# Performance work log

Measured on AMD Instinct MI355X. Metric: run time of the kernel, lower is better.

Reference implementation:

```python
import jax, jax.numpy as jnp
import numpy as np


def setup_inputs() -> dict:
    key = jax.random.key(0)
    k1, k2 = jax.random.split(key)
    B, N, M, K = 8, 4096, 4096, 64
    input1 = jax.random.normal(k1, (B, N, K), dtype=jnp.float32)
    input2 = jax.random.normal(k2, (B, M, K), dtype=jnp.float32)
    return {"input1": input1, "input2": input2}


def reference(input1, input2):
    # Pairwise L2 distances via the ||x||^2 + ||y||^2 - 2<x,y> identity,
    # avoiding the O(B*N*M*K) broadcast-subtraction intermediate.
    x2 = jnp.sum(input1 * input1, axis=-1)                 # [B, N]
    y2 = jnp.sum(input2 * input2, axis=-1)                 # [B, M]
    xy = jnp.einsum('bnk,bmk->bnm', input1, input2)        # [B, N, M]
    sq = x2[:, :, None] + y2[:, None, :] - 2.0 * xy
    D = jnp.sqrt(jnp.maximum(sq, 0.0))                     # [B, N, M]
    dist0 = jnp.mean(jnp.min(D, axis=1), axis=1)           # min over N, mean over M
    dist1 = jnp.mean(jnp.min(D, axis=2), axis=1)           # min over M, mean over N
    loss = jnp.mean(dist0 + dist1)
    return loss
```

## Files before the change

### kernel.cpp

```cpp
#include <hip/hip_runtime.h>

#define BATCH 8
#define NPTS  4096
#define KD    64
#define MQ    4
#define WALK  8
#define FINF  3.0e38f

typedef float f32x4 __attribute__((ext_vector_type(4)));
typedef float f32x2 __attribute__((ext_vector_type(2)));
typedef short s16x8 __attribute__((ext_vector_type(8)));

__device__ __forceinline__ unsigned int f2bf(float f) {
  unsigned int u = __float_as_uint(f);
  u += 0x7FFFu + ((u >> 16) & 1u);
  return u >> 16;
}

__device__ __forceinline__ void stage16(const void* g, void* l) {
  __builtin_amdgcn_global_load_lds((const __attribute__((address_space(1))) void*)g,
                                   (__attribute__((address_space(3))) void*)l, 16, 0, 0);
}

__global__ __launch_bounds__(256)
void prep_kernel(const float* __restrict__ X, const float* __restrict__ Y,
                 unsigned int* __restrict__ Xbf, unsigned int* __restrict__ Ybf,
                 float* __restrict__ x2, float* __restrict__ y2,
                 unsigned int* __restrict__ counter) {
  int gid = blockIdx.x * 256 + threadIdx.x;
  if (gid == 0) *counter = 0;
  int row = gid >> 5;
  int ki  = gid & 31;
  bool isX = row < BATCH * NPTS;
  int r2 = row & (BATCH * NPTS - 1);
  const float* src = isX ? X : Y;
  f32x2 v = *(const f32x2*)(src + (size_t)r2 * KD + ki * 2);
  float s = v[0] * v[0] + v[1] * v[1];
  #pragma unroll
  for (int m = 16; m >= 1; m >>= 1) s += __shfl_xor(s, m, 64);
  unsigned int packed = (f2bf(v[1]) << 16) | f2bf(v[0]);
  (isX ? Xbf : Ybf)[r2 * 32 + ki] = packed;
  if (ki == 0) (isX ? x2 : y2)[r2] = s;
}

__global__ __launch_bounds__(256, 2)
void chamfer_main(const unsigned short* __restrict__ Xbf,
                  const unsigned short* __restrict__ Ybf,
                  const float* __restrict__ x2g, const float* __restrict__ y2g,
                  float* __restrict__ rowpart,
                  float* __restrict__ colpart) {
  __shared__ __align__(16) unsigned short Ys[2][128 * 64];
  __shared__ float l_credq[2 * 4 * 132];
  __shared__ float l_redf[256];

  const int mq = blockIdx.x, ntile = blockIdx.y, b = blockIdx.z;
  const int n0 = ntile * 128;
  const int mbase = mq * (WALK * 128);
  const int t = threadIdx.x, w = t >> 6, lane = t & 63, c = lane & 15, q = lane >> 4;
  const int wr = (w >> 1) * 64, wc = (w & 1) * 64, rg = w >> 1;

  const int l8 = lane >> 3;
  const int lane_off = l8 * 128 + (((lane & 7) ^ l8) << 4);

  const unsigned short* Xrow = Xbf + (size_t)(b * NPTS + n0) * KD;
  const char* Yg0 = (const char*)(Ybf + (size_t)(b * NPTS + mbase) * KD);

  #pragma unroll
  for (int k = 0; k < 4; ++k)
    stage16(Yg0 + (k * 32 + w * 8) * 128 + lane_off,
            (char*)Ys[0] + (k * 256 + w * 64) * 16);

  s16x8 xf[4][2];
  #pragma unroll
  for (int i = 0; i < 4; ++i)
    #pragma unroll
    for (int ks = 0; ks < 2; ++ks)
      xf[i][ks] = *(const s16x8*)&Xrow[(size_t)(wr + i * 16 + c) * KD + (ks * 4 + q) * 8];

  const float* x2b = x2g + b * NPTS + n0;
  f32x4 x2r[4];
  #pragma unroll
  for (int i = 0; i < 4; ++i) x2r[i] = *(const f32x4*)(x2b + wr + i * 16 + q * 4);

  __syncthreads();

  float rm[4][4];
  #pragma unroll
  for (int i = 0; i < 4; ++i)
    #pragma unroll
    for (int r = 0; r < 4; ++r) rm[i][r] = FINF;

  const int cx = c & 7;
  const float* y2b = y2g + b * NPTS + mbase;
  float* colrow = colpart + (size_t)(ntile * 8 + b) * NPTS + mbase;
  const f32x4 zacc = {0.f, 0.f, 0.f, 0.f};

  #pragma unroll 2
  for (int tt = 0; tt < WALK; ++tt) {
    const unsigned short* cur = Ys[tt & 1];

    float y2c[4];
    #pragma unroll
    for (int j = 0; j < 4; ++j) y2c[j] = y2b[tt * 128 + wc + j * 16 + c];

    if (tt < WALK - 1) {
      const char* Ygt = Yg0 + (size_t)(tt + 1) * 128 * 128;
      unsigned short* nb = Ys[(tt + 1) & 1];
      #pragma unroll
      for (int k = 0; k < 4; ++k)
        stage16(Ygt + (k * 32 + w * 8) * 128 + lane_off,
                (char*)nb + (k * 256 + w * 64) * 16);
    }

    if (tt > 0 && t < 128) {
      int pt = tt - 1, pb = pt & 1;
      float v = fminf(fminf(l_credq[(pb * 4 + 0) * 132 + t], l_credq[(pb * 4 + 1) * 132 + t]),
                      fminf(l_credq[(pb * 4 + 2) * 132 + t], l_credq[(pb * 4 + 3) * 132 + t]));
      colrow[pt * 128 + t] = v + y2b[pt * 128 + t];
    }

    float cmj[4];
    #pragma unroll
    for (int j = 0; j < 4; ++j) {
      const unsigned short* yrow = &cur[(wc + j * 16 + c) * 64];
      s16x8 yf0 = *(const s16x8*)&yrow[(q ^ cx) << 3];
      s16x8 yf1 = *(const s16x8*)&yrow[((4 + q) ^ cx) << 3];
      f32x4 acc[4];
      #pragma unroll
      for (int i = 0; i < 4; ++i) {
        f32x4 a0 = __builtin_amdgcn_mfma_f32_16x16x32_bf16(xf[i][0], yf0, zacc, 0, 0, 0);
        acc[i] = __builtin_amdgcn_mfma_f32_16x16x32_bf16(xf[i][1], yf1, a0, 0, 0, 0);
      }
      float cm = FINF;
      #pragma unroll
      for (int i = 0; i < 4; ++i)
        #pragma unroll
        for (int r = 0; r < 4; ++r) {
          float v = acc[i][r];
          rm[i][r] = fminf(rm[i][r], fmaf(-2.f, v, y2c[j]));
          cm = fminf(cm, fmaf(-2.f, v, x2r[i][r]));
        }
      cm = fminf(cm, __shfl_xor(cm, 16, 64));
      cmj[j] = cm;
    }
    {
      int s = rg * 2 + (q >> 1);
      int jA = (q & 1) * 2;
      float sA = (q & 1) ? cmj[2] : cmj[0];
      float sB = (q & 1) ? cmj[3] : cmj[1];
      float* dst = &l_credq[((tt & 1) * 4 + s) * 132 + wc + c];
      dst[jA * 16]      = sA;
      dst[jA * 16 + 16] = sB;
    }

    __syncthreads();
  }

  #pragma unroll
  for (int msk = 1; msk <= 8; msk <<= 1)
    #pragma unroll
    for (int i = 0; i < 4; ++i)
      #pragma unroll
      for (int r = 0; r < 4; ++r)
        rm[i][r] = fminf(rm[i][r], __shfl_xor(rm[i][r], msk, 64));
  if (c == 0) {
    #pragma unroll
    for (int i = 0; i < 4; ++i) {
      f32x4 v = {rm[i][0], rm[i][1], rm[i][2], rm[i][3]};
      *(f32x4*)&l_redf[w * 64 + i * 16 + q * 4] = v;
    }
  }
  __syncthreads();

  if (t < 128) {
    {
      int pt = WALK - 1, pb = pt & 1;
      float v = fminf(fminf(l_credq[(pb * 4 + 0) * 132 + t], l_credq[(pb * 4 + 1) * 132 + t]),
                      fminf(l_credq[(pb * 4 + 2) * 132 + t], l_credq[(pb * 4 + 3) * 132 + t]));
      colrow[pt * 128 + t] = v + y2b[pt * 128 + t];
    }
    int g = t >> 6, lr = t & 63;
    float v = fminf(l_redf[(g * 2) * 64 + lr], l_redf[(g * 2 + 1) * 64 + lr]);
    rowpart[mq * (BATCH * NPTS) + b * NPTS + n0 + t] = v + x2b[t];
  }
}

__global__ __launch_bounds__(256)
void reduce_kernel(const float* __restrict__ rowpart, const float* __restrict__ colpart,
                   float* __restrict__ partials, unsigned int* __restrict__ counter,
                   float* __restrict__ out) {
  int i = blockIdx.x * 256 + threadIdx.x;
  const int TOT = BATCH * NPTS;
  float rv = FINF;
  #pragma unroll
  for (int s = 0; s < MQ; ++s) rv = fminf(rv, rowpart[s * TOT + i]);
  float s0 = sqrtf(fmaxf(rv, 0.f));
  float cv = FINF;
  #pragma unroll
  for (int nt = 0; nt < 32; ++nt) cv = fminf(cv, colpart[nt * TOT + i]);
  s0 += sqrtf(fmaxf(cv, 0.f));
  #pragma unroll
  for (int m = 32; m >= 1; m >>= 1) s0 += __shfl_xor(s0, m, 64);
  __shared__ float wsum[4];
  if ((threadIdx.x & 63) == 0) wsum[threadIdx.x >> 6] = s0;
  __syncthreads();

  if (threadIdx.x < 64) {
    unsigned int ticket = 0;
    if (threadIdx.x == 0) {
      float bsum = wsum[0] + wsum[1] + wsum[2] + wsum[3];
      atomicExch(&partials[blockIdx.x], bsum);
      __threadfence();
      ticket = atomicAdd(counter, 1);
    }
    ticket = __shfl(ticket, 0, 64);
    if (ticket == 127) {
      float v = atomicAdd(&partials[threadIdx.x], 0.0f) +
                atomicAdd(&partials[threadIdx.x + 64], 0.0f);
      #pragma unroll
      for (int m = 32; m >= 1; m >>= 1) v += __shfl_xor(v, m, 64);
      if (threadIdx.x == 0) out[0] = v * (1.0f / (float)TOT);
    }
  }
}

extern "C" void kernel_launch(void* const* d_in, const int* in_sizes, int n_in,
                              void* d_out, int out_size, void* d_ws, size_t ws_size,
                              hipStream_t stream) {
  const float* X = (const float*)d_in[0];
  const float* Y = (const float*)d_in[1];
  float* out = (float*)d_out;

  char* ws = (char*)d_ws;
  unsigned int* Xbf = (unsigned int*)ws;
  unsigned int* Ybf = (unsigned int*)(ws + (4u << 20));
  float* x2 = (float*)(ws + (8u << 20));
  float* y2 = (float*)(ws + (8u << 20) + (128u << 10));
  float* rowpart = (float*)(ws + (8u << 20) + (256u << 10));
  float* colpart = (float*)(ws + (9u << 20) + (256u << 10));
  float* partials = (float*)(ws + (13u << 20) + (256u << 10));
  unsigned int* counter = (unsigned int*)(partials + 128);

  prep_kernel<<<dim3(2 * BATCH * NPTS * 32 / 256), dim3(256), 0, stream>>>(
      X, Y, Xbf, Ybf, x2, y2, counter);

  chamfer_main<<<dim3(MQ, 32, 8), dim3(256), 0, stream>>>(
      (const unsigned short*)Xbf, (const unsigned short*)Ybf, x2, y2, rowpart, colpart);

  reduce_kernel<<<dim3(BATCH * NPTS / 256), dim3(256), 0, stream>>>(
      rowpart, colpart, partials, counter, out);
}
```

Before: 104.0 us.

## Replace partial-min buffers with global atomicMin and remap blocks for XCD locality

New measurement: 105.1 us. About the same (+1.0%).

```diff
diff --git a/kernel.cpp b/kernel.cpp
--- a/kernel.cpp
+++ b/kernel.cpp
@@ -26,9 +26,11 @@
 void prep_kernel(const float* __restrict__ X, const float* __restrict__ Y,
                  unsigned int* __restrict__ Xbf, unsigned int* __restrict__ Ybf,
                  float* __restrict__ x2, float* __restrict__ y2,
+                 unsigned int* __restrict__ minbuf,
                  unsigned int* __restrict__ counter) {
   int gid = blockIdx.x * 256 + threadIdx.x;
   if (gid == 0) *counter = 0;
+  if (gid < 2 * BATCH * NPTS) minbuf[gid] = 0x7F800000u;
   int row = gid >> 5;
   int ki  = gid & 31;
   bool isX = row < BATCH * NPTS;
@@ -47,13 +49,15 @@
 void chamfer_main(const unsigned short* __restrict__ Xbf,
                   const unsigned short* __restrict__ Ybf,
                   const float* __restrict__ x2g, const float* __restrict__ y2g,
-                  float* __restrict__ rowpart,
-                  float* __restrict__ colpart) {
+                  unsigned int* __restrict__ rowmin,
+                  unsigned int* __restrict__ colmin) {
   __shared__ __align__(16) unsigned short Ys[2][128 * 64];
   __shared__ float l_credq[2 * 4 * 132];
   __shared__ float l_redf[256];
 
-  const int mq = blockIdx.x, ntile = blockIdx.y, b = blockIdx.z;
+  const int lin = blockIdx.x;
+  const int logical = (lin & 7) * 128 + (lin >> 3);
+  const int mq = logical & 3, ntile = (logical >> 2) & 31, b = logical >> 7;
   const int n0 = ntile * 128;
   const int mbase = mq * (WALK * 128);
   const int t = threadIdx.x, w = t >> 6, lane = t & 63, c = lane & 15, q = lane >> 4;
@@ -92,7 +96,7 @@
 
   const int cx = c & 7;
   const float* y2b = y2g + b * NPTS + mbase;
-  float* colrow = colpart + (size_t)(ntile * 8 + b) * NPTS + mbase;
+  unsigned int* colbase = colmin + (size_t)b * NPTS + mbase;
   const f32x4 zacc = {0.f, 0.f, 0.f, 0.f};
 
   #pragma unroll 2
@@ -116,7 +120,8 @@
       int pt = tt - 1, pb = pt & 1;
       float v = fminf(fminf(l_credq[(pb * 4 + 0) * 132 + t], l_credq[(pb * 4 + 1) * 132 + t]),
                       fminf(l_credq[(pb * 4 + 2) * 132 + t], l_credq[(pb * 4 + 3) * 132 + t]));
-      colrow[pt * 128 + t] = v + y2b[pt * 128 + t];
+      float d = fmaxf(v + y2b[pt * 128 + t], 0.f);
+      atomicMin(&colbase[pt * 128 + t], __float_as_uint(d));
     }
 
     float cmj[4];
@@ -177,28 +182,23 @@
       int pt = WALK - 1, pb = pt & 1;
       float v = fminf(fminf(l_credq[(pb * 4 + 0) * 132 + t], l_credq[(pb * 4 + 1) * 132 + t]),
                       fminf(l_credq[(pb * 4 + 2) * 132 + t], l_credq[(pb * 4 + 3) * 132 + t]));
-      colrow[pt * 128 + t] = v + y2b[pt * 128 + t];
+      float d = fmaxf(v + y2b[pt * 128 + t], 0.f);
+      atomicMin(&colbase[pt * 128 + t], __float_as_uint(d));
     }
     int g = t >> 6, lr = t & 63;
-    float v = fminf(l_redf[(g * 2) * 64 + lr], l_redf[(g * 2 + 1) * 64 + lr]);
-    rowpart[mq * (BATCH * NPTS) + b * NPTS + n0 + t] = v + x2b[t];
+    float v = fminf(l_redf[(g * 2) * 64 + lr], l_redf[(g * 2 + 1) * 64 + lr]) + x2b[t];
+    atomicMin(&rowmin[(size_t)b * NPTS + n0 + t], __float_as_uint(fmaxf(v, 0.f)));
   }
 }
 
 __global__ __launch_bounds__(256)
-void reduce_kernel(const float* __restrict__ rowpart, const float* __restrict__ colpart,
+void reduce_kernel(const unsigned int* __restrict__ rowmin,
+                   const unsigned int* __restrict__ colmin,
                    float* __restrict__ partials, unsigned int* __restrict__ counter,
                    float* __restrict__ out) {
   int i = blockIdx.x * 256 + threadIdx.x;
   const int TOT = BATCH * NPTS;
-  float rv = FINF;
-  #pragma unroll
-  for (int s = 0; s < MQ; ++s) rv = fminf(rv, rowpart[s * TOT + i]);
-  float s0 = sqrtf(fmaxf(rv, 0.f));
-  float cv = FINF;
-  #pragma unroll
-  for (int nt = 0; nt < 32; ++nt) cv = fminf(cv, colpart[nt * TOT + i]);
-  s0 += sqrtf(fmaxf(cv, 0.f));
+  float s0 = sqrtf(__uint_as_float(rowmin[i])) + sqrtf(__uint_as_float(colmin[i]));
   #pragma unroll
   for (int m = 32; m >= 1; m >>= 1) s0 += __shfl_xor(s0, m, 64);
   __shared__ float wsum[4];
@@ -236,17 +236,18 @@
   unsigned int* Ybf = (unsigned int*)(ws + (4u << 20));
   float* x2 = (float*)(ws + (8u << 20));
   float* y2 = (float*)(ws + (8u << 20) + (128u << 10));
-  float* rowpart = (float*)(ws + (8u << 20) + (256u << 10));
-  float* colpart = (float*)(ws + (9u << 20) + (256u << 10));
-  float* partials = (float*)(ws + (13u << 20) + (256u << 10));
+  unsigned int* minbuf = (unsigned int*)(ws + (8u << 20) + (256u << 10));
+  unsigned int* rowmin = minbuf;
+  unsigned int* colmin = minbuf + BATCH * NPTS;
+  float* partials = (float*)(ws + (8u << 20) + (512u << 10));
   unsigned int* counter = (unsigned int*)(partials + 128);
 
   prep_kernel<<<dim3(2 * BATCH * NPTS * 32 / 256), dim3(256), 0, stream>>>(
-      X, Y, Xbf, Ybf, x2, y2, counter);
-
-  chamfer_main<<<dim3(MQ, 32, 8), dim3(256), 0, stream>>>(
-      (const unsigned short*)Xbf, (const unsigned short*)Ybf, x2, y2, rowpart, colpart);
+      X, Y, Xbf, Ybf, x2, y2, minbuf, counter);
+
+  chamfer_main<<<dim3(MQ * 32 * BATCH), dim3(256), 0, stream>>>(
+      (const unsigned short*)Xbf, (const unsigned short*)Ybf, x2, y2, rowmin, colmin);
 
   reduce_kernel<<<dim3(BATCH * NPTS / 256), dim3(256), 0, stream>>>(
-      rowpart, colpart, partials, counter, out);
-}
+      rowmin, colmin, partials, counter, out);
+}
```
